# Optimization experiments

Measured on AMD Instinct MI355X. Metric: run time of the kernel, lower is better.

Reference implementation:

```python
import jax, jax.numpy as jnp
import numpy as np

B, T, D, H = 2, 2048, 1024, 16
HD = D // H  # head_dim = 64


def setup_inputs() -> dict:
    key = jax.random.key(0)
    ks = jax.random.split(key, 5)
    s = 0.02
    return {
        "x": jax.random.normal(ks[0], (B, T, D), dtype=jnp.float32),
        "Wqkv": jax.random.normal(ks[1], (3 * D, D), dtype=jnp.float32) * s,
        "bqkv": jax.random.normal(ks[2], (3 * D,), dtype=jnp.float32) * s,
        "Wproj": jax.random.normal(ks[3], (D, D), dtype=jnp.float32) * s,
        "bproj": jax.random.normal(ks[4], (D,), dtype=jnp.float32) * s,
    }


def reference(x, Wqkv, bqkv, Wproj, bproj):
    b, t, d = x.shape
    qkv = x @ Wqkv.T + bqkv                      # [B,T,3D]
    q, k, v = jnp.split(qkv, 3, axis=-1)
    # [B,T,D] -> [B,H,T,HD]
    def to_heads(u):
        return u.reshape(b, t, H, HD).transpose(0, 2, 1, 3)
    q, k, v = to_heads(q), to_heads(k), to_heads(v)
    scale = 1.0 / jnp.sqrt(jnp.float32(HD))
    attn = jnp.einsum("bhqd,bhkd->bhqk", q, k) * scale   # [B,H,T,T]
    causal = jnp.tril(jnp.ones((t, t), dtype=bool))
    attn = jnp.where(causal[None, None, :, :], attn, -jnp.inf)
    attn = jax.nn.softmax(attn, axis=-1)
    scores = jnp.einsum("bhqk,bhkd->bhqd", attn, v)       # [B,H,T,HD]
    scores = scores.transpose(0, 2, 1, 3).reshape(b, t, d)
    return scores @ Wproj.T + bproj
```

## Files before the change

kernel.cpp:

```cpp
#include <hip/hip_runtime.h>

typedef __bf16 bf16_8 __attribute__((ext_vector_type(8)));
typedef __bf16 bf16_4 __attribute__((ext_vector_type(4)));
typedef float  f32_4  __attribute__((ext_vector_type(4)));

typedef __attribute__((address_space(1))) const void* as1_cvp;
typedef __attribute__((address_space(3))) void*       as3_vp;

__device__ __forceinline__ void load16_to_lds(const void* g, void* l) {
    __builtin_amdgcn_global_load_lds((as1_cvp)g, (as3_vp)l, 16, 0, 0);
}

__global__ __launch_bounds__(256) void cvt_all(
    const float* __restrict__ a, const float* __restrict__ b,
    const float* __restrict__ c, __bf16* __restrict__ out,
    int na4, int nb4, int nc4)
{
    int i = blockIdx.x * 256 + threadIdx.x;
    if (i >= na4 + nb4 + nc4) return;
    float4 f;
    if (i < na4)            f = ((const float4*)a)[i];
    else if (i < na4 + nb4) f = ((const float4*)b)[i - na4];
    else                    f = ((const float4*)c)[i - na4 - nb4];
    bf16_4 v = { (__bf16)f.x, (__bf16)f.y, (__bf16)f.z, (__bf16)f.w };
    ((bf16_4*)out)[i] = v;
}

#define BM 128
#define BK 32

template<int OUT_BF16, int BN_>
__global__ __launch_bounds__(256) void gemm_bt(
    const __bf16* __restrict__ A,
    const __bf16* __restrict__ B,
    const float*  __restrict__ bias,
    __bf16* __restrict__ Cb, float* __restrict__ Cf,
    int M, int N, int K)
{
    constexpr int NT = BN_ / 32;
    __shared__ __bf16 As[BM * BK];
    __shared__ __bf16 Bs[BN_ * BK];

    const int tid  = threadIdx.x;
    const int wave = tid >> 6;
    const int lane = tid & 63;
    const int wm = wave >> 1, wn = wave & 1;
    const int quad = lane >> 4, l16 = lane & 15;
    const int bm = blockIdx.y * BM, bn = blockIdx.x * BN_;

    const int srow = lane >> 2;
    const int scol = (lane & 3) * 8;

    f32_4 acc[4][NT];
    #pragma unroll
    for (int i = 0; i < 4; ++i)
        #pragma unroll
        for (int j = 0; j < NT; ++j)
            acc[i][j] = f32_4{0.f, 0.f, 0.f, 0.f};

    for (int k0 = 0; k0 < K; k0 += BK) {
        __syncthreads();
        #pragma unroll
        for (int p = 0; p < 2; ++p) {
            int r = 32 * wave + p * 16;
            load16_to_lds(A + (size_t)(bm + r + srow) * K + k0 + scol, &As[r * BK]);
        }
        if (BN_ == 128) {
            #pragma unroll
            for (int p = 0; p < 2; ++p) {
                int r = 32 * wave + p * 16;
                load16_to_lds(B + (size_t)(bn + r + srow) * K + k0 + scol, &Bs[r * BK]);
            }
        } else {
            int r = 16 * wave;
            load16_to_lds(B + (size_t)(bn + r + srow) * K + k0 + scol, &Bs[r * BK]);
        }
        __syncthreads();

        bf16_8 af[4], bfr[NT];
        #pragma unroll
        for (int mt = 0; mt < 4; ++mt)
            af[mt] = *(const bf16_8*)&As[(wm * 64 + mt * 16 + l16) * BK + quad * 8];
        #pragma unroll
        for (int nt = 0; nt < NT; ++nt)
            bfr[nt] = *(const bf16_8*)&Bs[(wn * (BN_/2) + nt * 16 + l16) * BK + quad * 8];
        #pragma unroll
        for (int mt = 0; mt < 4; ++mt)
            #pragma unroll
            for (int nt = 0; nt < NT; ++nt)
                acc[mt][nt] = __builtin_amdgcn_mfma_f32_16x16x32_bf16(
                    af[mt], bfr[nt], acc[mt][nt], 0, 0, 0);
    }

    #pragma unroll
    for (int mt = 0; mt < 4; ++mt) {
        #pragma unroll
        for (int nt = 0; nt < NT; ++nt) {
            int col = bn + wn * (BN_/2) + nt * 16 + l16;
            float bv = bias ? bias[col] : 0.f;
            #pragma unroll
            for (int r = 0; r < 4; ++r) {
                int row = bm + wm * 64 + mt * 16 + quad * 4 + r;
                float v = acc[mt][nt][r] + bv;
                if (OUT_BF16) Cb[(size_t)row * N + col] = (__bf16)v;
                else          Cf[(size_t)row * N + col] = v;
            }
        }
    }
}

__global__ __launch_bounds__(512) void attn_kernel(
    const __bf16* __restrict__ qkv, __bf16* __restrict__ out)
{
    constexpr int T = 2048;
    __shared__ __bf16 Ks[2][64 * 64];
    __shared__ __bf16 Vt[2][64 * 64];
    __shared__ __bf16 Ps[8][16 * 40];
    __shared__ float  Om[4][16 * 64];
    __shared__ float  Lm[4][16];

    const int tid  = threadIdx.x;
    const int wave = tid >> 6;
    const int lane = tid & 63;
    const int wg = wave >> 2, wq = wave & 3;
    const int quad = lane >> 4, l16 = lane & 15;
    const int z  = blockIdx.x;
    const int bh = blockIdx.y;
    const int b = bh >> 4, h = bh & 15;

    const size_t rowbase = (size_t)b * T;
    const __bf16* Kbase = qkv + 1024 + h * 64;
    const __bf16* Vbase = qkv + 2048 + h * 64;

    const int krow = tid >> 3;
    const int kcbs = tid & 7;
    const int kcbf = kcbs ^ (krow & 7);
    const int vrow = krow, va = kcbs;

    #pragma unroll
    for (int tile = 0; tile < 2; ++tile) {
        const int qt = tile ? (31 - z) : z;

        bf16_8 aq0, aq1;
        {
            const __bf16* qrow = qkv + (rowbase + qt * 64 + wq * 16 + l16) * 3072 + h * 64;
            aq0 = *(const bf16_8*)(qrow + quad * 8);
            aq1 = *(const bf16_8*)(qrow + 32 + quad * 8);
            #pragma unroll
            for (int u = 0; u < 8; ++u) {
                aq0[u] = (__bf16)((float)aq0[u] * 0.125f);
                aq1[u] = (__bf16)((float)aq1[u] * 0.125f);
            }
        }

        load16_to_lds(Kbase + (rowbase + krow) * 3072 + kcbf * 8, &Ks[0][wave * 512]);
        {
            bf16_8 vv = *(const bf16_8*)(Vbase + (rowbase + vrow) * 3072 + va * 8);
            int kc = vrow >> 3, kl = vrow & 7;
            #pragma unroll
            for (int u = 0; u < 8; ++u)
                Vt[0][(va * 8 + u) * 64 + ((kc ^ u ^ va) << 3) + kl] = vv[u];
        }

        float l_i[4];
        f32_4 O[4];
        #pragma unroll
        for (int r = 0; r < 4; ++r) l_i[r] = 0.f;
        #pragma unroll
        for (int dt = 0; dt < 4; ++dt) O[dt] = f32_4{0.f, 0.f, 0.f, 0.f};

        for (int j = 0; j <= qt; ++j) {
            const int cur = j & 1, nxt = cur ^ 1;
            __syncthreads();

            const int jn = j + 1;
            const bool stage = (jn <= qt);
            bf16_8 vv;
            if (stage) {
                load16_to_lds(Kbase + (rowbase + jn * 64 + krow) * 3072 + kcbf * 8,
                              &Ks[nxt][wave * 512]);
                vv = *(const bf16_8*)(Vbase + (rowbase + jn * 64 + vrow) * 3072 + va * 8);
            }

            f32_4 S[2];
            #pragma unroll
            for (int nt = 0; nt < 2; ++nt) {
                int rk = wg * 32 + nt * 16 + l16;
                int rx = rk & 7;
                bf16_8 kb0 = *(const bf16_8*)&Ks[cur][rk * 64 + ((quad ^ rx) << 3)];
                bf16_8 kb1 = *(const bf16_8*)&Ks[cur][rk * 64 + (((quad + 4) ^ rx) << 3)];
                f32_4 zz = {0.f, 0.f, 0.f, 0.f};
                zz = __builtin_amdgcn_mfma_f32_16x16x32_bf16(aq0, kb0, zz, 0, 0, 0);
                zz = __builtin_amdgcn_mfma_f32_16x16x32_bf16(aq1, kb1, zz, 0, 0, 0);
                S[nt] = zz;
            }

            #pragma unroll
            for (int r = 0; r < 4; ++r) {
                float p0 = __expf(S[0][r]);
                float p1 = __expf(S[1][r]);
                if (j == qt) {
                    int qloc = wq * 16 + quad * 4 + r;
                    if (wg * 32 + l16      > qloc) p0 = 0.f;
                    if (wg * 32 + 16 + l16 > qloc) p1 = 0.f;
                }
                l_i[r] += p0 + p1;
                Ps[wave][(quad * 4 + r) * 40 + l16]      = (__bf16)p0;
                Ps[wave][(quad * 4 + r) * 40 + 16 + l16] = (__bf16)p1;
            }

            bf16_8 ap = *(const bf16_8*)&Ps[wave][l16 * 40 + quad * 8];

            #pragma unroll
            for (int dt = 0; dt < 4; ++dt) {
                int d = dt * 16 + l16;
                int cb = (wg * 4 + quad) ^ (d & 7) ^ ((d >> 3) & 7);
                bf16_8 vb = *(const bf16_8*)&Vt[cur][d * 64 + (cb << 3)];
                O[dt] = __builtin_amdgcn_mfma_f32_16x16x32_bf16(ap, vb, O[dt], 0, 0, 0);
            }

            if (stage) {
                int kc = vrow >> 3, kl = vrow & 7;
                #pragma unroll
                for (int u = 0; u < 8; ++u)
                    Vt[nxt][(va * 8 + u) * 64 + ((kc ^ u ^ va) << 3) + kl] = vv[u];
            }
        }

        float lrow[4];
        #pragma unroll
        for (int r = 0; r < 4; ++r) {
            float v = l_i[r];
            #pragma unroll
            for (int off = 1; off <= 8; off <<= 1)
                v += __shfl_xor(v, off, 64);
            lrow[r] = v;
        }
        if (wg == 1) {
            #pragma unroll
            for (int r = 0; r < 4; ++r)
                #pragma unroll
                for (int dt = 0; dt < 4; ++dt)
                    Om[wq][(quad * 4 + r) * 64 + dt * 16 + l16] = O[dt][r];
            if (l16 == 0)
                #pragma unroll
                for (int r = 0; r < 4; ++r)
                    Lm[wq][quad * 4 + r] = lrow[r];
        }
        __syncthreads();
        if (wg == 0) {
            #pragma unroll
            for (int r = 0; r < 4; ++r) {
                float inv = 1.f / (lrow[r] + Lm[wq][quad * 4 + r]);
                int q = qt * 64 + wq * 16 + quad * 4 + r;
                #pragma unroll
                for (int dt = 0; dt < 4; ++dt) {
                    float val = (O[dt][r] + Om[wq][(quad * 4 + r) * 64 + dt * 16 + l16]) * inv;
                    out[(rowbase + q) * 1024 + h * 64 + dt * 16 + l16] = (__bf16)val;
                }
            }
        }
        __syncthreads();
    }
}

extern "C" void kernel_launch(void* const* d_in, const int* in_sizes, int n_in,
                              void* d_out, int out_size, void* d_ws, size_t ws_size,
                              hipStream_t stream)
{
    constexpr int Bc = 2, Tc = 2048, Dc = 1024;
    constexpr int M  = Bc * Tc;
    constexpr int N1 = 3 * Dc;

    const float* x     = (const float*)d_in[0];
    const float* Wqkv  = (const float*)d_in[1];
    const float* bqkv  = (const float*)d_in[2];
    const float* Wproj = (const float*)d_in[3];
    const float* bproj = (const float*)d_in[4];
    float* outp = (float*)d_out;

    __bf16* xb     = (__bf16*)d_ws;
    __bf16* wqkvb  = xb     + (size_t)M * Dc;
    __bf16* wprojb = wqkvb  + (size_t)N1 * Dc;
    __bf16* qkvb   = wprojb + (size_t)Dc * Dc;
    __bf16* attnb  = qkvb   + (size_t)M * N1;

    {
        int na4 = M * Dc / 4, nb4 = N1 * Dc / 4, nc4 = Dc * Dc / 4;
        int n4 = na4 + nb4 + nc4;
        cvt_all<<<(n4 + 255) / 256, 256, 0, stream>>>(x, Wqkv, Wproj, xb, na4, nb4, nc4);
    }

    gemm_bt<1, 128><<<dim3(N1 / 128, M / BM), 256, 0, stream>>>(
        xb, wqkvb, bqkv, qkvb, nullptr, M, N1, Dc);

    attn_kernel<<<dim3(16, Bc * 16), 512, 0, stream>>>(qkvb, attnb);

    gemm_bt<0, 64><<<dim3(Dc / 64, M / BM), 256, 0, stream>>>(
        attnb, wprojb, bproj, nullptr, outp, M, Dc, Dc);
}
```

Measured before the change: 192.0 us.

## Stage GEMM epilogue through LDS, load K to registers, remap attention grid per XCD

The GEMM epilogue now writes accumulators plus bias into an LDS tile and then issues coalesced 16-byte global stores, replacing scattered per-element stores. The attention kernel drops the K shared-memory buffer and has each wave load its K fragments straight into registers, prefetching the next tile. The launch becomes a 1-D grid whose block index is remapped so that blocks for the same batch-head land on the same XCD, aiming for better L2 reuse. Costs are an extra LDS round trip and barrier in the GEMM, more registers in attention, and K rows now read redundantly across the four query waves.

```diff
diff --git a/kernel.cpp b/kernel.cpp
--- a/kernel.cpp
+++ b/kernel.cpp
@@ -37,9 +37,11 @@
     __bf16* __restrict__ Cb, float* __restrict__ Cf,
     int M, int N, int K)
 {
-    constexpr int NT = BN_ / 32;
-    __shared__ __bf16 As[BM * BK];
-    __shared__ __bf16 Bs[BN_ * BK];
+    constexpr int NT   = BN_ / 32;
+    constexpr int CSTR = BN_ + (OUT_BF16 ? 8 : 4);
+    __shared__ __align__(16) char smem[35840];
+    __bf16* As = (__bf16*)smem;
+    __bf16* Bs = As + BM * BK;
 
     const int tid  = threadIdx.x;
     const int wave = tid >> 6;
@@ -92,19 +94,49 @@
                     af[mt], bfr[nt], acc[mt][nt], 0, 0, 0);
     }
 
-    #pragma unroll
-    for (int mt = 0; mt < 4; ++mt) {
-        #pragma unroll
-        for (int nt = 0; nt < NT; ++nt) {
-            int col = bn + wn * (BN_/2) + nt * 16 + l16;
-            float bv = bias ? bias[col] : 0.f;
-            #pragma unroll
-            for (int r = 0; r < 4; ++r) {
-                int row = bm + wm * 64 + mt * 16 + quad * 4 + r;
-                float v = acc[mt][nt][r] + bv;
-                if (OUT_BF16) Cb[(size_t)row * N + col] = (__bf16)v;
-                else          Cf[(size_t)row * N + col] = v;
-            }
+    __syncthreads();
+
+    if (OUT_BF16) {
+        __bf16* Cs = (__bf16*)smem;
+        #pragma unroll
+        for (int mt = 0; mt < 4; ++mt)
+            #pragma unroll
+            for (int nt = 0; nt < NT; ++nt) {
+                int col = wn * (BN_/2) + nt * 16 + l16;
+                float bv = bias ? bias[bn + col] : 0.f;
+                #pragma unroll
+                for (int r = 0; r < 4; ++r)
+                    Cs[(wm * 64 + mt * 16 + quad * 4 + r) * CSTR + col] =
+                        (__bf16)(acc[mt][nt][r] + bv);
+            }
+        __syncthreads();
+        const int rr = tid >> 4, cc = (tid & 15) * 8;
+        #pragma unroll
+        for (int p = 0; p < 8; ++p) {
+            int row = p * 16 + rr;
+            bf16_8 v = *(const bf16_8*)&Cs[row * CSTR + cc];
+            *(bf16_8*)(Cb + (size_t)(bm + row) * N + bn + cc) = v;
+        }
+    } else {
+        float* Cs = (float*)smem;
+        #pragma unroll
+        for (int mt = 0; mt < 4; ++mt)
+            #pragma unroll
+            for (int nt = 0; nt < NT; ++nt) {
+                int col = wn * (BN_/2) + nt * 16 + l16;
+                float bv = bias ? bias[bn + col] : 0.f;
+                #pragma unroll
+                for (int r = 0; r < 4; ++r)
+                    Cs[(wm * 64 + mt * 16 + quad * 4 + r) * CSTR + col] =
+                        acc[mt][nt][r] + bv;
+            }
+        __syncthreads();
+        const int rr = tid >> 4, cc = (tid & 15) * 4;
+        #pragma unroll
+        for (int p = 0; p < 8; ++p) {
+            int row = p * 16 + rr;
+            float4 v = *(const float4*)&Cs[row * CSTR + cc];
+            *(float4*)(Cf + (size_t)(bm + row) * N + bn + cc) = v;
         }
     }
 }
@@ -113,7 +145,6 @@
     const __bf16* __restrict__ qkv, __bf16* __restrict__ out)
 {
     constexpr int T = 2048;
-    __shared__ __bf16 Ks[2][64 * 64];
     __shared__ __bf16 Vt[2][64 * 64];
     __shared__ __bf16 Ps[8][16 * 40];
     __shared__ float  Om[4][16 * 64];
@@ -124,18 +155,19 @@
     const int lane = tid & 63;
     const int wg = wave >> 2, wq = wave & 3;
     const int quad = lane >> 4, l16 = lane & 15;
-    const int z  = blockIdx.x;
-    const int bh = blockIdx.y;
+
+    const int fid  = blockIdx.x;
+    const int xcd  = fid & 7;
+    const int loc  = fid >> 3;
+    const int bh   = xcd * 4 + (loc >> 4);
+    const int z    = loc & 15;
     const int b = bh >> 4, h = bh & 15;
 
     const size_t rowbase = (size_t)b * T;
     const __bf16* Kbase = qkv + 1024 + h * 64;
     const __bf16* Vbase = qkv + 2048 + h * 64;
 
-    const int krow = tid >> 3;
-    const int kcbs = tid & 7;
-    const int kcbf = kcbs ^ (krow & 7);
-    const int vrow = krow, va = kcbs;
+    const int vrow = tid >> 3, va = tid & 7;
 
     #pragma unroll
     for (int tile = 0; tile < 2; ++tile) {
@@ -153,7 +185,13 @@
             }
         }
 
-        load16_to_lds(Kbase + (rowbase + krow) * 3072 + kcbf * 8, &Ks[0][wave * 512]);
+        bf16_8 kf[2][2];
+        #pragma unroll
+        for (int nt = 0; nt < 2; ++nt) {
+            const __bf16* kr = Kbase + (rowbase + wg * 32 + nt * 16 + l16) * 3072;
+            kf[nt][0] = *(const bf16_8*)(kr + quad * 8);
+            kf[nt][1] = *(const bf16_8*)(kr + 32 + quad * 8);
+        }
         {
             bf16_8 vv = *(const bf16_8*)(Vbase + (rowbase + vrow) * 3072 + va * 8);
             int kc = vrow >> 3, kl = vrow & 7;
@@ -173,25 +211,25 @@
             const int cur = j & 1, nxt = cur ^ 1;
             __syncthreads();
 
-            const int jn = j + 1;
-            const bool stage = (jn <= qt);
-            bf16_8 vv;
+            const bool stage = (j < qt);
+            bf16_8 vv, kn[2][2];
             if (stage) {
-                load16_to_lds(Kbase + (rowbase + jn * 64 + krow) * 3072 + kcbf * 8,
-                              &Ks[nxt][wave * 512]);
+                const int jn = j + 1;
                 vv = *(const bf16_8*)(Vbase + (rowbase + jn * 64 + vrow) * 3072 + va * 8);
+                #pragma unroll
+                for (int nt = 0; nt < 2; ++nt) {
+                    const __bf16* kr = Kbase + (rowbase + jn * 64 + wg * 32 + nt * 16 + l16) * 3072;
+                    kn[nt][0] = *(const bf16_8*)(kr + quad * 8);
+                    kn[nt][1] = *(const bf16_8*)(kr + 32 + quad * 8);
+                }
             }
 
             f32_4 S[2];
             #pragma unroll
             for (int nt = 0; nt < 2; ++nt) {
-                int rk = wg * 32 + nt * 16 + l16;
-                int rx = rk & 7;
-                bf16_8 kb0 = *(const bf16_8*)&Ks[cur][rk * 64 + ((quad ^ rx) << 3)];
-                bf16_8 kb1 = *(const bf16_8*)&Ks[cur][rk * 64 + (((quad + 4) ^ rx) << 3)];
                 f32_4 zz = {0.f, 0.f, 0.f, 0.f};
-                zz = __builtin_amdgcn_mfma_f32_16x16x32_bf16(aq0, kb0, zz, 0, 0, 0);
-                zz = __builtin_amdgcn_mfma_f32_16x16x32_bf16(aq1, kb1, zz, 0, 0, 0);
+                zz = __builtin_amdgcn_mfma_f32_16x16x32_bf16(aq0, kf[nt][0], zz, 0, 0, 0);
+                zz = __builtin_amdgcn_mfma_f32_16x16x32_bf16(aq1, kf[nt][1], zz, 0, 0, 0);
                 S[nt] = zz;
             }
 
@@ -224,6 +262,11 @@
                 #pragma unroll
                 for (int u = 0; u < 8; ++u)
                     Vt[nxt][(va * 8 + u) * 64 + ((kc ^ u ^ va) << 3) + kl] = vv[u];
+                #pragma unroll
+                for (int nt = 0; nt < 2; ++nt) {
+                    kf[nt][0] = kn[nt][0];
+                    kf[nt][1] = kn[nt][1];
+                }
             }
         }
 
@@ -294,7 +337,7 @@
     gemm_bt<1, 128><<<dim3(N1 / 128, M / BM), 256, 0, stream>>>(
         xb, wqkvb, bqkv, qkvb, nullptr, M, N1, Dc);
 
-    attn_kernel<<<dim3(16, Bc * 16), 512, 0, stream>>>(qkvb, attnb);
+    attn_kernel<<<dim3(512), 512, 0, stream>>>(qkvb, attnb);
 
     gemm_bt<0, 64><<<dim3(Dc / 64, M / BM), 256, 0, stream>>>(
         attnb, wprojb, bproj, nullptr, outp, M, Dc, Dc);
```

Measured after the change: 227.7 us. 18.6% more time.
